# Kernel optimization log

Hardware: AMD Instinct MI355X
Metric: run time of the kernel (lower is better)

The kernel has to match this reference:

```python
import jax, jax.numpy as jnp
import numpy as np

N_EXPERTS, D_MODEL, D_FF, TOP_K, N_TOKENS = 8, 1024, 4096, 2, 8192

def _uniform_init(key, shape, fan_in):
    # matches torch init: gain = sqrt(1/3), std = gain/sqrt(fan_in), bound = sqrt(3)*std
    bound = np.sqrt(3.0) * np.sqrt(1.0 / 3.0) / np.sqrt(fan_in)
    return jax.random.uniform(key, shape, minval=-bound, maxval=bound, dtype=jnp.float32)

def setup_inputs() -> dict:
    key = jax.random.key(0)
    kx, ki, kw, k1, k2, k3 = jax.random.split(key, 6)
    x = jax.random.normal(kx, (N_TOKENS, D_MODEL), dtype=jnp.float32)
    expert_indices = jax.random.randint(ki, (N_TOKENS, TOP_K), 0, N_EXPERTS, dtype=jnp.int32)
    expert_weights = jax.random.uniform(kw, (N_TOKENS, TOP_K), dtype=jnp.float32)
    w1 = _uniform_init(k1, (N_EXPERTS, D_MODEL, D_FF), D_MODEL)
    w2 = _uniform_init(k2, (N_EXPERTS, D_MODEL, D_FF), D_MODEL)
    w3 = _uniform_init(k3, (N_EXPERTS, D_FF, D_MODEL), D_FF)
    return {"x": x, "expert_indices": expert_indices, "expert_weights": expert_weights,
            "w1": w1, "w2": w2, "w3": w3}

def reference(x, expert_indices, expert_weights, w1, w2, w3):
    # For each token t and routed expert e with routing weight p:
    #   out[t] += p * (silu(x[t] @ W1[e]) * (x[t] @ W2[e])) @ W3[e]
    # Loop over the small fixed expert set; compute each expert's SwiGLU FFN
    # densely over all tokens and combine with per-token routing weights
    # (mathematically identical to the sorted-dispatch grouped GEMM).
    n_experts = w1.shape[0]
    out = jnp.zeros_like(x)
    for e in range(n_experts):
        gate = x @ w1[e]                 # [N, d_ff]
        val = x @ w2[e]                  # [N, d_ff]
        y = (jax.nn.silu(gate) * val) @ w3[e]   # [N, d_model]
        # sum routing weights over top_k slots that picked expert e
        p = jnp.sum(jnp.where(expert_indices == e, expert_weights, 0.0), axis=1)
        out = out + p[:, None] * y
    return out
```

## Files before the change

kernel.cpp:

```cpp
#include <hip/hip_runtime.h>
#include <hip/hip_bf16.h>

typedef __attribute__((ext_vector_type(8))) short short8;
typedef __attribute__((ext_vector_type(4))) float f32x4;
typedef unsigned short u16;
typedef unsigned int u32;

#define NTOK   8192
#define DMODEL 1024
#define DFF    4096
#define NEXP   8
#define NPAIR  (NTOK * 2)
#define PADM   128
#define PPAD   (136 * 128)

#define OFF_XB   0ull
#define OFF_W1T  (OFF_XB  + (size_t)NTOK * DMODEL * 2)
#define OFF_W2T  (OFF_W1T + (size_t)NEXP * DFF * DMODEL * 2)
#define OFF_W3T  (OFF_W2T + (size_t)NEXP * DFF * DMODEL * 2)
#define OFF_H    (OFF_W3T + (size_t)NEXP * DMODEL * DFF * 2)
#define OFF_TOK  (OFF_H   + (size_t)PPAD * DFF * 2)
#define OFF_WGT  (OFF_TOK + (size_t)PPAD * 4)
#define OFF_OFFP (OFF_WGT + (size_t)PPAD * 4)
#define WS_END   (OFF_OFFP + 64)

#define GLOAD16(gp, lp)                                                        \
  __builtin_amdgcn_global_load_lds(                                            \
      (const __attribute__((address_space(1))) u32*)(gp),                      \
      (__attribute__((address_space(3))) u32*)(lp), 16, 0, 0)

__device__ __forceinline__ u16 f2bu(float f) {
  __hip_bfloat16 b = __float2bfloat16(f);
  return __builtin_bit_cast(u16, b);
}


__global__ __launch_bounds__(256) void cvt_x_k(const float* __restrict__ x,
                                               u16* __restrict__ xb) {
  int i = blockIdx.x * 256 + threadIdx.x;
  float4 v = ((const float4*)x)[i];
  unsigned long long pk = (unsigned long long)f2bu(v.x) |
                          ((unsigned long long)f2bu(v.y) << 16) |
                          ((unsigned long long)f2bu(v.z) << 32) |
                          ((unsigned long long)f2bu(v.w) << 48);
  ((unsigned long long*)xb)[i] = pk;
}

__global__ __launch_bounds__(256) void wcvt_k(const float* __restrict__ w1,
                                              const float* __restrict__ w2,
                                              const float* __restrict__ w3,
                                              u16* __restrict__ w1t,
                                              u16* __restrict__ w2t,
                                              u16* __restrict__ w3t) {
  const int z = blockIdx.y;
  const float* src; u16* dst; int R, C, tx, ty;
  if (z < 16) {
    R = DMODEL; C = DFF;
    int e = z & 7;
    src = ((z < 8) ? w1 : w2) + (size_t)e * R * C;
    dst = ((z < 8) ? w1t : w2t) + (size_t)e * R * C;
    tx = blockIdx.x & 63; ty = blockIdx.x >> 6;
  } else {
    R = DFF; C = DMODEL;
    int e = z - 16;
    src = w3 + (size_t)e * R * C;
    dst = w3t + (size_t)e * R * C;
    tx = blockIdx.x & 15; ty = blockIdx.x >> 4;
  }
  const int c0 = tx * 64, r0 = ty * 256;
  __shared__ u16 t[256][68];
  const int tid = threadIdx.x;
  const int cl = (tid & 15) * 4, rl = tid >> 4;
#pragma unroll
  for (int p = 0; p < 16; ++p) {
    int r = rl + p * 16;
    float4 v = *(const float4*)(src + (size_t)(r0 + r) * C + c0 + cl);
    unsigned long long pk = (unsigned long long)f2bu(v.x) |
                            ((unsigned long long)f2bu(v.y) << 16) |
                            ((unsigned long long)f2bu(v.z) << 32) |
                            ((unsigned long long)f2bu(v.w) << 48);
    *(unsigned long long*)&t[r][cl] = pk;
  }
  __syncthreads();
  const int c = tid >> 2, seg = tid & 3;
#pragma unroll
  for (int u = 0; u < 8; ++u) {
    int rbase = seg * 8 + u * 32;
    short8 o;
#pragma unroll
    for (int j = 0; j < 8; ++j) o[j] = (short)t[rbase + j][c];
    *(short8*)(dst + (size_t)(c0 + c) * R + r0 + rbase) = o;
  }
}


__global__ __launch_bounds__(1024) void route_k(const int* __restrict__ ei,
                                                const float* __restrict__ ew,
                                                int* __restrict__ tok,
                                                float* __restrict__ wg,
                                                int* __restrict__ offp_g) {
  __shared__ int cnt[NEXP], offp[NEXP + 1], cur[NEXP];
  const int tid = threadIdx.x;
  if (tid < NEXP) { cnt[tid] = 0; cur[tid] = 0; }
  __syncthreads();
  for (int i = tid; i < PPAD; i += 1024) { tok[i] = 0; wg[i] = 0.f; }
  for (int i = tid; i < NPAIR; i += 1024) {
    int e = ei[i];
#pragma unroll
    for (int x = 0; x < NEXP; ++x) {
      unsigned long long m = __ballot(e == x);
      if ((tid & 63) == 0 && m) atomicAdd(&cnt[x], (int)__popcll(m));
    }
  }
  __syncthreads();
  if (tid == 0) {
    int a = 0;
#pragma unroll
    for (int e = 0; e < NEXP; ++e) { offp[e] = a; a += (cnt[e] + PADM - 1) & ~(PADM - 1); }
    offp[NEXP] = a;
  }
  __syncthreads();
  for (int i = tid; i < NPAIR; i += 1024) {
    int e = ei[i];
    int p = offp[e] + atomicAdd(&cur[e], 1);
    tok[p] = i >> 1;
    wg[p] = ew[i];
  }
  if (tid <= NEXP) offp_g[tid] = offp[tid];
}


#define S1_BUF 12288
#define S1_NK  32

__global__ __launch_bounds__(512, 4) void stage1_k(const u16* __restrict__ xb,
                                                   const u16* __restrict__ w1t,
                                                   const u16* __restrict__ w2t,
                                                   u16* __restrict__ h,
                                                   const int* __restrict__ tok,
                                                   const int* __restrict__ offp) {
  extern __shared__ __align__(16) u16 lds[];
  const int r0 = blockIdx.y * 128;
  if (r0 >= offp[NEXP]) return;
  int e = 0;
#pragma unroll
  for (int q = 0; q < 7; ++q) e += (offp[e + 1] <= r0) ? 1 : 0;
  const int n0 = blockIdx.x * 128;
  const int tid = threadIdx.x;
  const int lane = tid & 63, w = tid >> 6;
  const int wm = w >> 2, wn = w & 3;

  const int sl = lane & 3, rl = lane >> 2;
  const u16* aga;
  int adb;
  {
    int row = w * 16 + rl;
    int t = tok[r0 + row];
    aga = xb + (size_t)t * DMODEL + ((sl ^ ((row >> 1) & 3)) << 3);
    adb = (w * 16) * 32;
  }
  const u16* w1e = w1t + (size_t)e * DFF * DMODEL;
  const u16* w2e = w2t + (size_t)e * DFF * DMODEL;
  const u16* bg1; const u16* bg2;
  int bdb;
  {
    int row = w * 16 + rl;
    size_t ro = (size_t)(n0 + row) * DMODEL + ((sl ^ ((row >> 1) & 3)) << 3);
    bg1 = w1e + ro; bg2 = w2e + ro;
    bdb = (w * 16) * 32;
  }

  int aoff[4], boff[2];
  {
    int ks = lane >> 4;
#pragma unroll
    for (int mi = 0; mi < 4; ++mi) {
      int row = wm * 64 + mi * 16 + (lane & 15);
      aoff[mi] = row * 32 + ((ks ^ ((row >> 1) & 3)) << 3);
    }
#pragma unroll
    for (int ni = 0; ni < 2; ++ni) {
      int col = wn * 32 + ni * 16 + (lane & 15);
      boff[ni] = col * 32 + ((ks ^ ((col >> 1) & 3)) << 3);
    }
  }

  f32x4 accg[4][2], accv[4][2];
  const f32x4 zero = {0.f, 0.f, 0.f, 0.f};
#pragma unroll
  for (int mi = 0; mi < 4; ++mi)
#pragma unroll
    for (int ni = 0; ni < 2; ++ni) { accg[mi][ni] = zero; accv[mi][ni] = zero; }

#define S1_ISSUE(Q, KO)                                                        \
  do {                                                                         \
    GLOAD16(aga + (KO), (Q) + adb);                                            \
    GLOAD16(bg1 + (KO), (Q) + 4096 + bdb);                                     \
    GLOAD16(bg2 + (KO), (Q) + 8192 + bdb);                                     \
  } while (0)

  S1_ISSUE(lds, 0);
  S1_ISSUE(lds + S1_BUF, 32);
  asm volatile("s_waitcnt vmcnt(3)" ::: "memory");
  __builtin_amdgcn_s_barrier();
  __builtin_amdgcn_sched_barrier(0);

#define S1_STEP(P, KC, ISSUE)                                                  \
  {                                                                            \
    const u16* Ab  = lds + (P) * S1_BUF;                                       \
    const u16* B1b = Ab + 4096;                                                \
    const u16* B2b = Ab + 8192;                                                \
    short8 af[4], b1f[2], b2f[2];                                              \
    _Pragma("unroll") for (int mi = 0; mi < 4; ++mi)                           \
      af[mi] = *(const short8*)(Ab + aoff[mi]);                                \
    _Pragma("unroll") for (int ni = 0; ni < 2; ++ni) {                         \
      b1f[ni] = *(const short8*)(B1b + boff[ni]);                              \
      b2f[ni] = *(const short8*)(B2b + boff[ni]);                              \
    }                                                                          \
    if (ISSUE) S1_ISSUE(lds + (((P) + 2) % 3) * S1_BUF, ((KC) + 2) * 32);      \
    __builtin_amdgcn_s_setprio(1);                                             \
    _Pragma("unroll") for (int mi = 0; mi < 4; ++mi)                           \
      _Pragma("unroll") for (int ni = 0; ni < 2; ++ni) {                       \
        accg[mi][ni] = __builtin_amdgcn_mfma_f32_16x16x32_bf16(                \
            af[mi], b1f[ni], accg[mi][ni], 0, 0, 0);                           \
        accv[mi][ni] = __builtin_amdgcn_mfma_f32_16x16x32_bf16(                \
            af[mi], b2f[ni], accv[mi][ni], 0, 0, 0);                           \
      }                                                                        \
    __builtin_amdgcn_s_setprio(0);                                             \
    if (ISSUE) asm volatile("s_waitcnt vmcnt(3)" ::: "memory");                \
    else       asm volatile("s_waitcnt vmcnt(0)" ::: "memory");                \
    __builtin_amdgcn_s_barrier();                                              \
    __builtin_amdgcn_sched_barrier(0);                                         \
  }

  for (int kc = 0; kc < S1_NK - 2; kc += 3) {
    S1_STEP(0, kc, 1)
    S1_STEP(1, kc + 1, 1)
    S1_STEP(2, kc + 2, 1)
  }
  S1_STEP(0, S1_NK - 2, 0)
  S1_STEP(1, S1_NK - 1, 0)
#undef S1_STEP
#undef S1_ISSUE

  const int prow = r0 + wm * 64 + ((lane >> 4) << 2);
  const int pcol = n0 + wn * 32 + (lane & 15);
#pragma unroll
  for (int mi = 0; mi < 4; ++mi)
#pragma unroll
    for (int ni = 0; ni < 2; ++ni)
#pragma unroll
      for (int j = 0; j < 4; ++j) {
        float g = accg[mi][ni][j];
        float v = accv[mi][ni][j];
        float s = g / (1.f + __expf(-g));
        h[(size_t)(prow + mi * 16 + j) * DFF + (pcol + ni * 16)] = f2bu(s * v);
      }
}


#define S2_BUF 12288
#define S2_NK  128

__global__ __launch_bounds__(512, 4) void stage2_k(const u16* __restrict__ h,
                                                   const u16* __restrict__ w3t,
                                                   float* __restrict__ out,
                                                   const int* __restrict__ tok,
                                                   const float* __restrict__ wg,
                                                   const int* __restrict__ offp) {
  extern __shared__ __align__(16) u16 lds[];
  const int orig = blockIdx.y * 4 + blockIdx.x;
  const int wgid = (orig & 7) * 68 + (orig >> 3);
  const int bx = wgid & 3, by = wgid >> 2;
  const int r0 = by * 128;
  if (r0 >= offp[NEXP]) return;
  int e = 0;
#pragma unroll
  for (int q = 0; q < 7; ++q) e += (offp[e + 1] <= r0) ? 1 : 0;
  const int n0 = bx * 256;
  const int tid = threadIdx.x;
  const int lane = tid & 63, w = tid >> 6;
  const int wm = w >> 2, wn = w & 3;

  const int sl = lane & 3, rl = lane >> 2;
  const u16* aga;
  int adb;
  {
    int row = w * 16 + rl;
    aga = h + (size_t)(r0 + row) * DFF + ((sl ^ ((row >> 1) & 3)) << 3);
    adb = (w * 16) * 32;
  }
  const u16* w3e = w3t + (size_t)e * DMODEL * DFF;
  const u16* bga[2];
  int bdb[2];
#pragma unroll
  for (int j = 0; j < 2; ++j) {
    int row = w * 32 + j * 16 + rl;
    bga[j] = w3e + (size_t)(n0 + row) * DFF + ((sl ^ ((row >> 1) & 3)) << 3);
    bdb[j] = 4096 + (w * 32 + j * 16) * 32;
  }

  int aoff[4], boff[4];
  {
    int ks = lane >> 4;
#pragma unroll
    for (int mi = 0; mi < 4; ++mi) {
      int row = wm * 64 + mi * 16 + (lane & 15);
      aoff[mi] = row * 32 + ((ks ^ ((row >> 1) & 3)) << 3);
    }
#pragma unroll
    for (int ni = 0; ni < 4; ++ni) {
      int col = wn * 64 + ni * 16 + (lane & 15);
      boff[ni] = 4096 + col * 32 + ((ks ^ ((col >> 1) & 3)) << 3);
    }
  }

  f32x4 acc[4][4];
  const f32x4 zero = {0.f, 0.f, 0.f, 0.f};
#pragma unroll
  for (int mi = 0; mi < 4; ++mi)
#pragma unroll
    for (int ni = 0; ni < 4; ++ni) acc[mi][ni] = zero;

#define S2_ISSUE(Q, KO)                                                        \
  do {                                                                         \
    GLOAD16(aga + (KO), (Q) + adb);                                            \
    GLOAD16(bga[0] + (KO), (Q) + bdb[0]);                                      \
    GLOAD16(bga[1] + (KO), (Q) + bdb[1]);                                      \
  } while (0)

  S2_ISSUE(lds, 0);
  S2_ISSUE(lds + S2_BUF, 32);
  asm volatile("s_waitcnt vmcnt(3)" ::: "memory");
  __builtin_amdgcn_s_barrier();
  __builtin_amdgcn_sched_barrier(0);

#define S2_STEP(P, KC, ISSUE)                                                  \
  {                                                                            \
    const u16* Qb = lds + (P) * S2_BUF;                                        \
    short8 af[4], bf[4];                                                       \
    _Pragma("unroll") for (int mi = 0; mi < 4; ++mi)                           \
      af[mi] = *(const short8*)(Qb + aoff[mi]);                                \
    _Pragma("unroll") for (int ni = 0; ni < 4; ++ni)                           \
      bf[ni] = *(const short8*)(Qb + boff[ni]);                                \
    if (ISSUE) S2_ISSUE(lds + (((P) + 2) % 3) * S2_BUF, ((KC) + 2) * 32);      \
    __builtin_amdgcn_s_setprio(1);                                             \
    _Pragma("unroll") for (int mi = 0; mi < 4; ++mi)                           \
      _Pragma("unroll") for (int ni = 0; ni < 4; ++ni)                         \
        acc[mi][ni] = __builtin_amdgcn_mfma_f32_16x16x32_bf16(                 \
            af[mi], bf[ni], acc[mi][ni], 0, 0, 0);                             \
    __builtin_amdgcn_s_setprio(0);                                             \
    if (ISSUE) asm volatile("s_waitcnt vmcnt(3)" ::: "memory");                \
    else       asm volatile("s_waitcnt vmcnt(0)" ::: "memory");                \
    __builtin_amdgcn_s_barrier();                                              \
    __builtin_amdgcn_sched_barrier(0);                                         \
  }

  for (int kc = 0; kc < S2_NK - 2; kc += 3) {
    S2_STEP(0, kc, 1)
    S2_STEP(1, kc + 1, 1)
    S2_STEP(2, kc + 2, 1)
  }
  S2_STEP(0, S2_NK - 2, 0)
  S2_STEP(1, S2_NK - 1, 0)
#undef S2_STEP
#undef S2_ISSUE

  const int prow = r0 + wm * 64 + ((lane >> 4) << 2);
  const int pcolb = n0 + wn * 64 + (lane & 15);
#pragma unroll
  for (int mi = 0; mi < 4; ++mi)
#pragma unroll
    for (int j = 0; j < 4; ++j) {
      int pos = prow + mi * 16 + j;
      float p = wg[pos];
      if (p != 0.f) {
        int t = tok[pos];
#pragma unroll
        for (int ni = 0; ni < 4; ++ni)
          atomicAdd(&out[(size_t)t * DMODEL + pcolb + ni * 16], p * acc[mi][ni][j]);
      }
    }
}


extern "C" void kernel_launch(void* const* d_in, const int* in_sizes, int n_in,
                              void* d_out, int out_size, void* d_ws, size_t ws_size,
                              hipStream_t stream) {
  (void)in_sizes; (void)n_in;
  const float* x  = (const float*)d_in[0];
  const int*   ei = (const int*)d_in[1];
  const float* ew = (const float*)d_in[2];
  const float* w1 = (const float*)d_in[3];
  const float* w2 = (const float*)d_in[4];
  const float* w3 = (const float*)d_in[5];
  float* out = (float*)d_out;
  char* ws = (char*)d_ws;

  hipMemsetAsync(out, 0, (size_t)out_size * sizeof(float), stream);
  if (ws_size < WS_END) return;

  u16* xb   = (u16*)(ws + OFF_XB);
  u16* w1t  = (u16*)(ws + OFF_W1T);
  u16* w2t  = (u16*)(ws + OFF_W2T);
  u16* w3t  = (u16*)(ws + OFF_W3T);
  u16* hb   = (u16*)(ws + OFF_H);
  int* tok  = (int*)(ws + OFF_TOK);
  float* wg = (float*)(ws + OFF_WGT);
  int* offp = (int*)(ws + OFF_OFFP);

  hipFuncSetAttribute(reinterpret_cast<const void*>(stage1_k),
                      hipFuncAttributeMaxDynamicSharedMemorySize, 73728);
  hipFuncSetAttribute(reinterpret_cast<const void*>(stage2_k),
                      hipFuncAttributeMaxDynamicSharedMemorySize, 73728);

  cvt_x_k<<<dim3(NTOK * DMODEL / 4 / 256), 256, 0, stream>>>(x, xb);
  wcvt_k<<<dim3(256, 24), 256, 0, stream>>>(w1, w2, w3, w1t, w2t, w3t);
  route_k<<<dim3(1), 1024, 0, stream>>>(ei, ew, tok, wg, offp);
  stage1_k<<<dim3(DFF / 128, PPAD / 128), 512, 73728, stream>>>(xb, w1t, w2t, hb, tok, offp);
  stage2_k<<<dim3(DMODEL / 256, PPAD / 128), 512, 73728, stream>>>(hb, w3t, out, tok, wg, offp);
}
```

Before: 691.8 us.

## Replace atomic scatter-add with per-pair stores and a deterministic gather reduce

```diff
diff --git a/kernel.cpp b/kernel.cpp
--- a/kernel.cpp
+++ b/kernel.cpp
@@ -22,7 +22,9 @@
 #define OFF_TOK  (OFF_H   + (size_t)PPAD * DFF * 2)
 #define OFF_WGT  (OFF_TOK + (size_t)PPAD * 4)
 #define OFF_OFFP (OFF_WGT + (size_t)PPAD * 4)
-#define WS_END   (OFF_OFFP + 64)
+#define OFF_INV  (OFF_OFFP + 64)
+#define WS_END   (OFF_INV + (size_t)NPAIR * 4)
+#define OFF_PH   OFF_W1T
 
 #define GLOAD16(gp, lp)                                                        \
   __builtin_amdgcn_global_load_lds(                                            \
@@ -98,7 +100,8 @@
                                                 const float* __restrict__ ew,
                                                 int* __restrict__ tok,
                                                 float* __restrict__ wg,
-                                                int* __restrict__ offp_g) {
+                                                int* __restrict__ offp_g,
+                                                int* __restrict__ inv) {
   __shared__ int cnt[NEXP], offp[NEXP + 1], cur[NEXP];
   const int tid = threadIdx.x;
   if (tid < NEXP) { cnt[tid] = 0; cur[tid] = 0; }
@@ -125,6 +128,7 @@
     int p = offp[e] + atomicAdd(&cur[e], 1);
     tok[p] = i >> 1;
     wg[p] = ew[i];
+    inv[i] = p;
   }
   if (tid <= NEXP) offp_g[tid] = offp[tid];
 }
@@ -264,8 +268,7 @@
 
 __global__ __launch_bounds__(512, 4) void stage2_k(const u16* __restrict__ h,
                                                    const u16* __restrict__ w3t,
-                                                   float* __restrict__ out,
-                                                   const int* __restrict__ tok,
+                                                   float* __restrict__ ph,
                                                    const float* __restrict__ wg,
                                                    const int* __restrict__ offp) {
   extern __shared__ __align__(16) u16 lds[];
@@ -374,13 +377,23 @@
     for (int j = 0; j < 4; ++j) {
       int pos = prow + mi * 16 + j;
       float p = wg[pos];
-      if (p != 0.f) {
-        int t = tok[pos];
-#pragma unroll
-        for (int ni = 0; ni < 4; ++ni)
-          atomicAdd(&out[(size_t)t * DMODEL + pcolb + ni * 16], p * acc[mi][ni][j]);
-      }
-    }
+#pragma unroll
+      for (int ni = 0; ni < 4; ++ni)
+        ph[(size_t)pos * DMODEL + pcolb + ni * 16] = p * acc[mi][ni][j];
+    }
+}
+
+
+__global__ __launch_bounds__(256) void reduce_k(const float* __restrict__ ph,
+                                                const int* __restrict__ inv,
+                                                float* __restrict__ out) {
+  const int t = blockIdx.x;
+  const int s0 = inv[t * 2], s1 = inv[t * 2 + 1];
+  const float4* p0 = (const float4*)(ph + (size_t)s0 * DMODEL);
+  const float4* p1 = (const float4*)(ph + (size_t)s1 * DMODEL);
+  float4 a = p0[threadIdx.x], b = p1[threadIdx.x];
+  float4 r; r.x = a.x + b.x; r.y = a.y + b.y; r.z = a.z + b.z; r.w = a.w + b.w;
+  ((float4*)(out + (size_t)t * DMODEL))[threadIdx.x] = r;
 }
 
 
@@ -408,6 +421,8 @@
   int* tok  = (int*)(ws + OFF_TOK);
   float* wg = (float*)(ws + OFF_WGT);
   int* offp = (int*)(ws + OFF_OFFP);
+  int* inv  = (int*)(ws + OFF_INV);
+  float* ph = (float*)(ws + OFF_PH);
 
   hipFuncSetAttribute(reinterpret_cast<const void*>(stage1_k),
                       hipFuncAttributeMaxDynamicSharedMemorySize, 73728);
@@ -416,7 +431,8 @@
 
   cvt_x_k<<<dim3(NTOK * DMODEL / 4 / 256), 256, 0, stream>>>(x, xb);
   wcvt_k<<<dim3(256, 24), 256, 0, stream>>>(w1, w2, w3, w1t, w2t, w3t);
-  route_k<<<dim3(1), 1024, 0, stream>>>(ei, ew, tok, wg, offp);
+  route_k<<<dim3(1), 1024, 0, stream>>>(ei, ew, tok, wg, offp, inv);
   stage1_k<<<dim3(DFF / 128, PPAD / 128), 512, 73728, stream>>>(xb, w1t, w2t, hb, tok, offp);
-  stage2_k<<<dim3(DMODEL / 256, PPAD / 128), 512, 73728, stream>>>(hb, w3t, out, tok, wg, offp);
-}
+  stage2_k<<<dim3(DMODEL / 256, PPAD / 128), 512, 73728, stream>>>(hb, w3t, ph, wg, offp);
+  reduce_k<<<dim3(NTOK), 256, 0, stream>>>(ph, inv, out);
+}
```

Result: slower. 779.8 us (+12.7%).
